# Kernel tuning notes

Hardware: AMD Instinct MI355X
Metric: run time of the kernel (lower is better)

Reference implementation:

```python
import jax, jax.numpy as jnp
import numpy as np

N_WIRES = 12
BLOCK_CONFIGS = [(12, 3), (12, 3)]
HAM_OFFSET = 0.0
HAM_COEFF = 1.0
BATCH = 4096


def _sq(psi, w):
    # view statevector (B, 2^n) as (B, left, 2, right) isolating wire w
    B = psi.shape[0]
    n = N_WIRES
    return psi.reshape(B, 1 << w, 2, 1 << (n - 1 - w))


def _rx(psi, theta, w):
    s = _sq(psi, w)
    t = jnp.asarray(theta, jnp.float32).reshape(-1, 1, 1, 1) * 0.5
    out = jnp.cos(t) * s - 1j * jnp.sin(t) * jnp.flip(s, axis=2)
    return out.reshape(psi.shape)


def _ry(psi, theta, w):
    # [[c,-s],[s,c]]: new = cos*psi + sin*sgn*flip(psi), sgn = (-1, +1)
    s = _sq(psi, w)
    t = jnp.asarray(theta, jnp.float32).reshape(-1, 1, 1, 1) * 0.5
    sgn = jnp.array([-1.0, 1.0], jnp.float32).reshape(1, 1, 2, 1)
    out = jnp.cos(t) * s + jnp.sin(t) * sgn * jnp.flip(s, axis=2)
    return out.reshape(psi.shape)


def _rz(psi, theta, w):
    # diag(e^{-i t/2}, e^{+i t/2})
    s = _sq(psi, w)
    t = jnp.asarray(theta, jnp.float32).reshape(-1, 1, 1, 1) * 0.5
    z = jnp.array([-1.0, 1.0], jnp.float32).reshape(1, 1, 2, 1)
    out = s * jnp.exp(1j * (t * z).astype(jnp.complex64))
    return out.reshape(psi.shape)


def _cnot(psi, c, t):
    B = psi.shape[0]
    n = N_WIRES
    lo, hi = (c, t) if c < t else (t, c)
    s = psi.reshape(B, 1 << lo, 2, 1 << (hi - lo - 1), 2, 1 << (n - 1 - hi))
    ctrl_ax = 2 if c == lo else 4
    tgt_ax = 4 if c == lo else 2
    p0 = jax.lax.index_in_dim(s, 0, axis=ctrl_ax, keepdims=True)
    p1 = jnp.flip(jax.lax.index_in_dim(s, 1, axis=ctrl_ax, keepdims=True), axis=tgt_ax)
    out = jnp.concatenate([p0, p1], axis=ctrl_ax)
    return out.reshape(psi.shape)


def setup_inputs() -> dict:
    key = jax.random.key(0)
    k1, k2 = jax.random.split(key)
    total_encode = sum(ne for ne, _ in BLOCK_CONFIGS)
    total_ansatz = sum(ld for _, ld in BLOCK_CONFIGS)
    x = jax.random.normal(k1, (BATCH, total_encode), dtype=jnp.float32)
    ansatz_weights = jax.random.uniform(
        k2, (total_ansatz, 3, N_WIRES), dtype=jnp.float32,
        minval=-np.pi, maxval=np.pi)
    return {"x": x, "ansatz_weights": ansatz_weights}


def reference(x, ansatz_weights):
    B = x.shape[0]
    n = N_WIRES
    psi = jnp.zeros((B, 1 << n), jnp.complex64).at[:, 0].set(1.0)
    param_col = 0
    ansatz_block = 0
    for n_encode, linear_depth in BLOCK_CONFIGS:
        for j in range(n_encode):
            wire = j % n
            if param_col < x.shape[1]:
                psi = _rx(psi, x[:, param_col], wire)
            param_col += 1
        for _ in range(linear_depth):
            w = ansatz_weights[ansatz_block]
            for i in range(n):
                psi = _ry(psi, w[0, i], i)
                psi = _rz(psi, w[1, i], i)
                psi = _ry(psi, w[2, i], i)
            for i in range(n):
                psi = _cnot(psi, i, (i + 1) % n)
            ansatz_block += 1
    # <H> with H = offset + coeff * sum_i Z_i : diagonal = n - 2*popcount(k)
    probs = psi.real ** 2 + psi.imag ** 2
    k = jnp.arange(1 << n)
    pop = ((k[:, None] >> jnp.arange(n)[None, :]) & 1).sum(-1).astype(jnp.float32)
    diag = HAM_OFFSET + HAM_COEFF * (n - 2.0 * pop)
    expval = probs @ diag  # (B,)
    return expval[:, None]
```

## Files before the change

### kernel.cpp

```cpp
#include <hip/hip_runtime.h>
#include <math.h>

#define NT 256
#define NS 4096

typedef float f32x2 __attribute__((ext_vector_type(2)));

constexpr int ring_pi_c(int k) {
    int u = k ^ (k >> 1);
    u ^= u >> 2; u ^= u >> 4; u ^= u >> 8;
    int w0 = ((u >> 11) ^ u) & 1;
    return (u & 0x7FF) | (w0 << 11);
}
constexpr int sig2(int m) { return m ^ ((m >> 4) & 0xF) ^ ((m >> 8) & 0xF); }

__device__ __forceinline__ void app1p(f32x2 ab, f32x2 cd, f32x2& a0, f32x2& a1) {
    f32x2 n0, n1;
    asm("v_pk_mul_f32 %0, %2, %4 op_sel:[0,0] op_sel_hi:[1,0]\n\t"
        "v_pk_fma_f32 %0, %2, %4, %0 op_sel:[1,1,0] op_sel_hi:[0,1,1] neg_hi:[0,1,0]\n\t"
        "v_pk_fma_f32 %0, %3, %5, %0 op_sel:[0,0,0] op_sel_hi:[1,0,1] neg_lo:[0,1,0] neg_hi:[0,1,0]\n\t"
        "v_pk_fma_f32 %0, %3, %5, %0 op_sel:[1,1,0] op_sel_hi:[0,1,1] neg_lo:[0,1,0]\n\t"
        "v_pk_mul_f32 %1, %3, %4 op_sel:[0,0] op_sel_hi:[1,0]\n\t"
        "v_pk_fma_f32 %1, %3, %4, %1 op_sel:[1,1,0] op_sel_hi:[0,1,1] neg_lo:[0,1,0]\n\t"
        "v_pk_fma_f32 %1, %2, %5, %1 op_sel:[0,0,0] op_sel_hi:[1,0,1]\n\t"
        "v_pk_fma_f32 %1, %2, %5, %1 op_sel:[1,1,0] op_sel_hi:[0,1,1] neg_lo:[0,1,0]"
        : "=&v"(n0), "=&v"(n1)
        : "v"(a0), "v"(a1), "v"(ab), "v"(cd));
    a0 = n0; a1 = n1;
}

template<int P>
__device__ __forceinline__ void gate_on_bit(f32x2 a[16], f32x2 ab, f32x2 cd) {
    #pragma unroll
    for (int r = 0; r < 16; ++r)
        if (!(r & (1 << P)))
            app1p(ab, cd, a[r], a[r | (1 << P)]);
}

__global__ __launch_bounds__(NT, 2)
void tqhea_kernel(const float* __restrict__ x,
                  const float* __restrict__ wts,
                  float* __restrict__ out)
{
    __shared__ f32x2  psi[NS];
    __shared__ float4 U[72];
    __shared__ float2 rxcs[12];
    __shared__ float  redbuf[4];

    const int b = blockIdx.x;
    const int t = threadIdx.x;

    if (t < 72) {
        int ab = t / 12, w = t % 12;
        float a  = 0.5f * wts[(ab * 3 + 0) * 12 + w];
        float bb = 0.5f * wts[(ab * 3 + 1) * 12 + w];
        float g  = 0.5f * wts[(ab * 3 + 2) * 12 + w];
        float sa, ca, sb, cb, sg, cg;
        sincosf(a,  &sa, &ca);
        sincosf(bb, &sb, &cb);
        sincosf(g,  &sg, &cg);
        float A = cb * (ca * cg - sa * sg);
        float B = sb * (ca * cg + sa * sg);
        float C = cb * (sa * cg + ca * sg);
        float D = sb * (sa * cg - ca * sg);
        if (ab == 3) {
            float th = 0.5f * x[b * 24 + 12 + w];
            float s, c; sincosf(th, &s, &c);
            float A2 = A*c + D*s, B2 = B*c - C*s, C2 = C*c + B*s, D2 = D*c - A*s;
            A = A2; B = B2; C = C2; D = D2;
        }
        U[t] = make_float4(A, B, C, D);
    }
    if (t < 12) {
        float th = 0.5f * x[b * 24 + t];
        float s, c; sincosf(th, &s, &c);
        rxcs[t] = make_float2(c, s);
    }
    __syncthreads();

    const int lo = t & 0xF, h = t >> 4;
    const int tb     = (t & 0xF0) | (lo ^ h);
    const int baseP1 = (h << 8) | (lo ^ h);
    const int baseP2 = (t << 4) | (lo ^ h);
    const int Qt     = sig2(ring_pi_c(t << 4));
    const int Pt     = ring_pi_c(t << 4);

    {
        float mlo = 1.f;
        #pragma unroll
        for (int bit = 0; bit < 8; ++bit)
            mlo *= ((t >> bit) & 1) ? rxcs[11 - bit].y : rxcs[11 - bit].x;
        int pct = __popc(t);
        #pragma unroll
        for (int r = 0; r < 16; ++r) {
            float mhi = 1.f;
            #pragma unroll
            for (int p = 0; p < 4; ++p)
                mhi *= ((r >> p) & 1) ? rxcs[3 - p].y : rxcs[3 - p].x;
            float mag = mhi * mlo;
            int pc = (pct + __popc(r)) & 3;
            f32x2 v;
            v.x = (pc == 0) ? mag : ((pc == 2) ? -mag : 0.f);
            v.y = (pc == 1) ? -mag : ((pc == 3) ? mag : 0.f);
            psi[(r << 8) | (tb ^ r)] = v;
        }
    }
    __syncthreads();

    float acc = 0.f;

    #pragma unroll 1
    for (int l = 0; l < 6; ++l) {
        f32x2 a[16];
        f32x2 gab, gcd;
        #pragma unroll
        for (int r = 0; r < 16; ++r) a[r] = psi[(r << 8) | (tb ^ r)];
        { float4 g = U[l*12+0]; gab = f32x2{g.x,g.y}; gcd = f32x2{g.z,g.w}; gate_on_bit<3>(a, gab, gcd); }
        { float4 g = U[l*12+1]; gab = f32x2{g.x,g.y}; gcd = f32x2{g.z,g.w}; gate_on_bit<2>(a, gab, gcd); }
        { float4 g = U[l*12+2]; gab = f32x2{g.x,g.y}; gcd = f32x2{g.z,g.w}; gate_on_bit<1>(a, gab, gcd); }
        { float4 g = U[l*12+3]; gab = f32x2{g.x,g.y}; gcd = f32x2{g.z,g.w}; gate_on_bit<0>(a, gab, gcd); }
        #pragma unroll
        for (int r = 0; r < 16; ++r) psi[(r << 8) | (tb ^ r)] = a[r];
        __syncthreads();

        #pragma unroll
        for (int r = 0; r < 16; ++r) a[r] = psi[baseP1 ^ (17 * r)];
        { float4 g = U[l*12+4]; gab = f32x2{g.x,g.y}; gcd = f32x2{g.z,g.w}; gate_on_bit<3>(a, gab, gcd); }
        { float4 g = U[l*12+5]; gab = f32x2{g.x,g.y}; gcd = f32x2{g.z,g.w}; gate_on_bit<2>(a, gab, gcd); }
        { float4 g = U[l*12+6]; gab = f32x2{g.x,g.y}; gcd = f32x2{g.z,g.w}; gate_on_bit<1>(a, gab, gcd); }
        { float4 g = U[l*12+7]; gab = f32x2{g.x,g.y}; gcd = f32x2{g.z,g.w}; gate_on_bit<0>(a, gab, gcd); }
        #pragma unroll
        for (int r = 0; r < 16; ++r) psi[baseP1 ^ (17 * r)] = a[r];
        __syncthreads();

        #pragma unroll
        for (int r = 0; r < 16; ++r) a[r] = psi[baseP2 ^ r];
        if (l < 5) __syncthreads();
        { float4 g = U[l*12+8];  gab = f32x2{g.x,g.y}; gcd = f32x2{g.z,g.w}; gate_on_bit<3>(a, gab, gcd); }
        { float4 g = U[l*12+9];  gab = f32x2{g.x,g.y}; gcd = f32x2{g.z,g.w}; gate_on_bit<2>(a, gab, gcd); }
        { float4 g = U[l*12+10]; gab = f32x2{g.x,g.y}; gcd = f32x2{g.z,g.w}; gate_on_bit<1>(a, gab, gcd); }
        { float4 g = U[l*12+11]; gab = f32x2{g.x,g.y}; gcd = f32x2{g.z,g.w}; gate_on_bit<0>(a, gab, gcd); }
        if (l < 5) {
            #pragma unroll
            for (int r = 0; r < 16; ++r)
                psi[Qt ^ sig2(ring_pi_c(r))] = a[r];
            __syncthreads();
        } else {
            #pragma unroll
            for (int r = 0; r < 16; ++r) {
                float d = 12.0f - 2.0f * (float)__popc(Pt ^ ring_pi_c(r));
                acc += (a[r].x * a[r].x + a[r].y * a[r].y) * d;
            }
        }
    }

    #pragma unroll
    for (int off = 32; off > 0; off >>= 1)
        acc += __shfl_down(acc, off);
    int wid = t >> 6, lane = t & 63;
    if (lane == 0) redbuf[wid] = acc;
    __syncthreads();
    if (t == 0) out[b] = redbuf[0] + redbuf[1] + redbuf[2] + redbuf[3];
}

extern "C" void kernel_launch(void* const* d_in, const int* in_sizes, int n_in,
                              void* d_out, int out_size, void* d_ws, size_t ws_size,
                              hipStream_t stream) {
    const float* x   = (const float*)d_in[0];
    const float* wts = (const float*)d_in[1];
    float* out = (float*)d_out;
    int B = in_sizes[0] / 24;
    tqhea_kernel<<<dim3(B), dim3(NT), 0, stream>>>(x, wts, out);
}
```

Before: 211.1 us.

## Precompute gate matrices in prep kernel and raise occupancy target

A separate prep kernel now computes the 72 fused ansatz gate matrices once, along with the per-sample RX cos/sin values. The batch kernel loads these from global memory and folds in the block-3 encoding rotation on the fly. This removes the per-block trig prologue, a barrier, and the shared-memory U/rxcs arrays. It also reuses psi shared memory for the reduction and raises launch_bounds to 5 blocks per SM, at the cost of an extra launch, global/scalar loads inside the gate loop, and tighter register limits.

New measurement: 250.3 us. +18.6%, slower.

```diff
diff --git a/kernel.cpp b/kernel.cpp
--- a/kernel.cpp
+++ b/kernel.cpp
@@ -37,21 +37,35 @@
             app1p(ab, cd, a[r], a[r | (1 << P)]);
 }
 
-__global__ __launch_bounds__(NT, 2)
-void tqhea_kernel(const float* __restrict__ x,
-                  const float* __restrict__ wts,
-                  float* __restrict__ out)
+__device__ __forceinline__ void load_gate(const float4* __restrict__ Uw,
+                                          const float2* __restrict__ cs12,
+                                          int l, int w, bool fold,
+                                          f32x2& ab, f32x2& cd) {
+    float4 g = Uw[l * 12 + w];
+    float A = g.x, B = g.y, C = g.z, D = g.w;
+    if (fold) {
+        float2 sc = cs12[w];
+        float c = sc.x, s = sc.y;
+        float A2 = A*c + D*s, B2 = B*c - C*s, C2 = C*c + B*s, D2 = D*c - A*s;
+        A = A2; B = B2; C = C2; D = D2;
+    }
+    ab = f32x2{A, B}; cd = f32x2{C, D};
+}
+
+__global__ void prep_kernel(const float* __restrict__ x,
+                            const float* __restrict__ wts,
+                            float4* __restrict__ Uw,
+                            float2* __restrict__ cs,
+                            int total)
 {
-    __shared__ f32x2  psi[NS];
-    __shared__ float4 U[72];
-    __shared__ float2 rxcs[12];
-    __shared__ float  redbuf[4];
-
-    const int b = blockIdx.x;
-    const int t = threadIdx.x;
-
-    if (t < 72) {
-        int ab = t / 12, w = t % 12;
+    int idx = blockIdx.x * blockDim.x + threadIdx.x;
+    if (idx < total) {
+        float th = 0.5f * x[idx];
+        float s, c; sincosf(th, &s, &c);
+        cs[idx] = make_float2(c, s);
+    }
+    if (idx < 72) {
+        int ab = idx / 12, w = idx % 12;
         float a  = 0.5f * wts[(ab * 3 + 0) * 12 + w];
         float bb = 0.5f * wts[(ab * 3 + 1) * 12 + w];
         float g  = 0.5f * wts[(ab * 3 + 2) * 12 + w];
@@ -63,20 +77,19 @@
         float B = sb * (ca * cg + sa * sg);
         float C = cb * (sa * cg + ca * sg);
         float D = sb * (sa * cg - ca * sg);
-        if (ab == 3) {
-            float th = 0.5f * x[b * 24 + 12 + w];
-            float s, c; sincosf(th, &s, &c);
-            float A2 = A*c + D*s, B2 = B*c - C*s, C2 = C*c + B*s, D2 = D*c - A*s;
-            A = A2; B = B2; C = C2; D = D2;
-        }
-        U[t] = make_float4(A, B, C, D);
-    }
-    if (t < 12) {
-        float th = 0.5f * x[b * 24 + t];
-        float s, c; sincosf(th, &s, &c);
-        rxcs[t] = make_float2(c, s);
-    }
-    __syncthreads();
+        Uw[idx] = make_float4(A, B, C, D);
+    }
+}
+
+__global__ __launch_bounds__(NT, 5)
+void tqhea_kernel(const float4* __restrict__ Uw,
+                  const float2* __restrict__ cs,
+                  float* __restrict__ out)
+{
+    __shared__ f32x2 psi[NS];
+
+    const int b = blockIdx.x;
+    const int t = threadIdx.x;
 
     const int lo = t & 0xF, h = t >> 4;
     const int tb     = (t & 0xF0) | (lo ^ h);
@@ -85,18 +98,24 @@
     const int Qt     = sig2(ring_pi_c(t << 4));
     const int Pt     = ring_pi_c(t << 4);
 
+    const float2* csb  = cs + b * 24;
+    const float2* cs12 = csb + 12;
+
     {
+        float2 rc[12];
+        #pragma unroll
+        for (int i = 0; i < 12; ++i) rc[i] = csb[i];
         float mlo = 1.f;
         #pragma unroll
         for (int bit = 0; bit < 8; ++bit)
-            mlo *= ((t >> bit) & 1) ? rxcs[11 - bit].y : rxcs[11 - bit].x;
+            mlo *= ((t >> bit) & 1) ? rc[11 - bit].y : rc[11 - bit].x;
         int pct = __popc(t);
         #pragma unroll
         for (int r = 0; r < 16; ++r) {
             float mhi = 1.f;
             #pragma unroll
             for (int p = 0; p < 4; ++p)
-                mhi *= ((r >> p) & 1) ? rxcs[3 - p].y : rxcs[3 - p].x;
+                mhi *= ((r >> p) & 1) ? rc[3 - p].y : rc[3 - p].x;
             float mag = mhi * mlo;
             int pc = (pct + __popc(r)) & 3;
             f32x2 v;
@@ -111,24 +130,26 @@
 
     #pragma unroll 1
     for (int l = 0; l < 6; ++l) {
+        const bool fold = (l == 3);
         f32x2 a[16];
         f32x2 gab, gcd;
+
         #pragma unroll
         for (int r = 0; r < 16; ++r) a[r] = psi[(r << 8) | (tb ^ r)];
-        { float4 g = U[l*12+0]; gab = f32x2{g.x,g.y}; gcd = f32x2{g.z,g.w}; gate_on_bit<3>(a, gab, gcd); }
-        { float4 g = U[l*12+1]; gab = f32x2{g.x,g.y}; gcd = f32x2{g.z,g.w}; gate_on_bit<2>(a, gab, gcd); }
-        { float4 g = U[l*12+2]; gab = f32x2{g.x,g.y}; gcd = f32x2{g.z,g.w}; gate_on_bit<1>(a, gab, gcd); }
-        { float4 g = U[l*12+3]; gab = f32x2{g.x,g.y}; gcd = f32x2{g.z,g.w}; gate_on_bit<0>(a, gab, gcd); }
+        load_gate(Uw, cs12, l, 0, fold, gab, gcd); gate_on_bit<3>(a, gab, gcd);
+        load_gate(Uw, cs12, l, 1, fold, gab, gcd); gate_on_bit<2>(a, gab, gcd);
+        load_gate(Uw, cs12, l, 2, fold, gab, gcd); gate_on_bit<1>(a, gab, gcd);
+        load_gate(Uw, cs12, l, 3, fold, gab, gcd); gate_on_bit<0>(a, gab, gcd);
         #pragma unroll
         for (int r = 0; r < 16; ++r) psi[(r << 8) | (tb ^ r)] = a[r];
         __syncthreads();
 
         #pragma unroll
         for (int r = 0; r < 16; ++r) a[r] = psi[baseP1 ^ (17 * r)];
-        { float4 g = U[l*12+4]; gab = f32x2{g.x,g.y}; gcd = f32x2{g.z,g.w}; gate_on_bit<3>(a, gab, gcd); }
-        { float4 g = U[l*12+5]; gab = f32x2{g.x,g.y}; gcd = f32x2{g.z,g.w}; gate_on_bit<2>(a, gab, gcd); }
-        { float4 g = U[l*12+6]; gab = f32x2{g.x,g.y}; gcd = f32x2{g.z,g.w}; gate_on_bit<1>(a, gab, gcd); }
-        { float4 g = U[l*12+7]; gab = f32x2{g.x,g.y}; gcd = f32x2{g.z,g.w}; gate_on_bit<0>(a, gab, gcd); }
+        load_gate(Uw, cs12, l, 4, fold, gab, gcd); gate_on_bit<3>(a, gab, gcd);
+        load_gate(Uw, cs12, l, 5, fold, gab, gcd); gate_on_bit<2>(a, gab, gcd);
+        load_gate(Uw, cs12, l, 6, fold, gab, gcd); gate_on_bit<1>(a, gab, gcd);
+        load_gate(Uw, cs12, l, 7, fold, gab, gcd); gate_on_bit<0>(a, gab, gcd);
         #pragma unroll
         for (int r = 0; r < 16; ++r) psi[baseP1 ^ (17 * r)] = a[r];
         __syncthreads();
@@ -136,10 +157,10 @@
         #pragma unroll
         for (int r = 0; r < 16; ++r) a[r] = psi[baseP2 ^ r];
         if (l < 5) __syncthreads();
-        { float4 g = U[l*12+8];  gab = f32x2{g.x,g.y}; gcd = f32x2{g.z,g.w}; gate_on_bit<3>(a, gab, gcd); }
-        { float4 g = U[l*12+9];  gab = f32x2{g.x,g.y}; gcd = f32x2{g.z,g.w}; gate_on_bit<2>(a, gab, gcd); }
-        { float4 g = U[l*12+10]; gab = f32x2{g.x,g.y}; gcd = f32x2{g.z,g.w}; gate_on_bit<1>(a, gab, gcd); }
-        { float4 g = U[l*12+11]; gab = f32x2{g.x,g.y}; gcd = f32x2{g.z,g.w}; gate_on_bit<0>(a, gab, gcd); }
+        load_gate(Uw, cs12, l, 8,  fold, gab, gcd); gate_on_bit<3>(a, gab, gcd);
+        load_gate(Uw, cs12, l, 9,  fold, gab, gcd); gate_on_bit<2>(a, gab, gcd);
+        load_gate(Uw, cs12, l, 10, fold, gab, gcd); gate_on_bit<1>(a, gab, gcd);
+        load_gate(Uw, cs12, l, 11, fold, gab, gcd); gate_on_bit<0>(a, gab, gcd);
         if (l < 5) {
             #pragma unroll
             for (int r = 0; r < 16; ++r)
@@ -157,10 +178,13 @@
     #pragma unroll
     for (int off = 32; off > 0; off >>= 1)
         acc += __shfl_down(acc, off);
-    int wid = t >> 6, lane = t & 63;
-    if (lane == 0) redbuf[wid] = acc;
     __syncthreads();
-    if (t == 0) out[b] = redbuf[0] + redbuf[1] + redbuf[2] + redbuf[3];
+    if ((t & 63) == 0) ((float*)psi)[t >> 6] = acc;
+    __syncthreads();
+    if (t == 0) {
+        const float* rb = (const float*)psi;
+        out[b] = rb[0] + rb[1] + rb[2] + rb[3];
+    }
 }
 
 extern "C" void kernel_launch(void* const* d_in, const int* in_sizes, int n_in,
@@ -170,5 +194,11 @@
     const float* wts = (const float*)d_in[1];
     float* out = (float*)d_out;
     int B = in_sizes[0] / 24;
-    tqhea_kernel<<<dim3(B), dim3(NT), 0, stream>>>(x, wts, out);
-}
+
+    float4* Uw = (float4*)d_ws;
+    float2* cs = (float2*)((char*)d_ws + 1152);
+    int total = B * 24;
+
+    prep_kernel<<<dim3((total + NT - 1) / NT), dim3(NT), 0, stream>>>(x, wts, Uw, cs, total);
+    tqhea_kernel<<<dim3(B), dim3(NT), 0, stream>>>(Uw, cs, out);
+}
```
